# Performance work log

Measured on AMD Instinct MI355X. Metric: run time of the kernel, lower is better.

Reference implementation:

```python
import jax, jax.numpy as jnp
import numpy as np
import math

B, S, KV, D, H = 4, 512, 4096, 1024, 16
HD = D // H  # head_dim = 64


def setup_inputs() -> dict:
    key = jax.random.key(0)
    ks = jax.random.split(key, 12)
    scale = 0.02
    return {
        "x": jax.random.normal(ks[0], (B, S, D), dtype=jnp.float32),
        "xa": jax.random.normal(ks[1], (B, KV, D), dtype=jnp.float32),
        "Wq": jax.random.normal(ks[2], (D, D), dtype=jnp.float32) * scale,
        "bq": jax.random.normal(ks[3], (D,), dtype=jnp.float32) * scale,
        "Wk": jax.random.normal(ks[4], (D, D), dtype=jnp.float32) * scale,  # key has no bias
        "Wv": jax.random.normal(ks[5], (D, D), dtype=jnp.float32) * scale,
        "bv": jax.random.normal(ks[6], (D,), dtype=jnp.float32) * scale,
        "Wo": jax.random.normal(ks[7], (D, D), dtype=jnp.float32) * scale,
        "bo": jax.random.normal(ks[8], (D,), dtype=jnp.float32) * scale,
        "cache_k": jnp.zeros((B, H, KV, HD), dtype=jnp.float32),
        "cache_v": jnp.zeros((B, H, KV, HD), dtype=jnp.float32),
    }


def reference(x, xa, Wq, bq, Wk, Wv, bv, Wo, bo, cache_k, cache_v):
    bsz, seq_len, _ = x.shape
    kv_len = xa.shape[1]
    # projections (torch nn.Linear convention: y = x @ W^T + b)
    q = (x @ Wq.T + bq).reshape(bsz, seq_len, H, HD).transpose(0, 2, 1, 3)   # [B,H,S,HD]
    k = (xa @ Wk.T).reshape(bsz, kv_len, H, HD).transpose(0, 2, 1, 3)        # [B,H,KV,HD]
    v = (xa @ Wv.T + bv).reshape(bsz, kv_len, H, HD).transpose(0, 2, 1, 3)   # [B,H,KV,HD]
    # prefill path: scatter k/v into positions [0, kv_len) of the cache
    updated_k = cache_k.at[:, :, :kv_len, :].set(k)
    updated_v = cache_v.at[:, :, :kv_len, :].set(v)
    # attention over full cache, fp32 softmax as in the original
    scores = jnp.einsum('bhqd,bhkd->bhqk', q, updated_k) / math.sqrt(HD)
    probs = jax.nn.softmax(scores.astype(jnp.float32), axis=-1).astype(q.dtype)
    attn = jnp.einsum('bhqk,bhkd->bhqd', probs, updated_v)                   # [B,H,S,HD]
    attn = attn.transpose(0, 2, 1, 3).reshape(bsz, seq_len, H * HD)
    out = attn @ Wo.T + bo
    return out, updated_k, updated_v
```

## Files before the change

kernel.cpp:

```cpp
#include <hip/hip_runtime.h>
#include <hip/hip_bf16.h>

using u16 = unsigned short;
typedef __bf16 bf16x8 __attribute__((ext_vector_type(8)));
typedef float f32x4 __attribute__((ext_vector_type(4)));

#define SB 4
#define SS 512
#define SKV 4096
#define SD 1024
#define SH 16
#define SHD 64
#define NSPLIT 4
#define NROWS 32768

__device__ inline u16 f2bf(float f){
  __hip_bfloat16 h = __float2bfloat16(f);
  return __builtin_bit_cast(u16, h);
}

__device__ inline bf16x8 ld_frag_g(const u16* p){
  uint4 v = *reinterpret_cast<const uint4*>(p);
  return __builtin_bit_cast(bf16x8, v);
}

__device__ inline bf16x8 ld_frag_lds(const char* base, int ob){
  uint4 v = *reinterpret_cast<const uint4*>(base + ob);
  return __builtin_bit_cast(bf16x8, v);
}

__device__ inline void gload_lds16(const u16* g, u16* l){
  __builtin_amdgcn_global_load_lds(
      (const __attribute__((address_space(1))) void*)g,
      (__attribute__((address_space(3))) void*)l, 16, 0, 0);
}

__global__ __launch_bounds__(256) void cast_kernel(const float* __restrict__ src,
                                                   u16* __restrict__ dst, int n4){
  int i = blockIdx.x * 256 + threadIdx.x;
  if (i < n4){
    float4 f = reinterpret_cast<const float4*>(src)[i];
    ushort4 u;
    u.x = f2bf(f.x); u.y = f2bf(f.y); u.z = f2bf(f.z); u.w = f2bf(f.w);
    reinterpret_cast<ushort4*>(dst)[i] = u;
  }
}

enum { MODE_Q = 0, MODE_K = 1, MODE_V = 2, MODE_OUT = 3 };

template<int MODE>
__global__ __launch_bounds__(256) void gemm_bt(const u16* __restrict__ A,
                                               const u16* __restrict__ W,
                                               const float* __restrict__ bias,
                                               float* __restrict__ outF,
                                               u16* __restrict__ outB)
{
  __shared__ u16 As[128*64];
  __shared__ u16 Bs[128*64];
  const int tid  = threadIdx.x;
  const int lane = tid & 63;
  const int wm   = ((tid >> 6) >> 1) * 64;
  const int wn   = ((tid >> 6) & 1) * 64;
  const long rowBase = (long)blockIdx.x * 128;
  const long colBase = (long)blockIdx.y * 128;

  f32x4 acc[4][4];
#pragma unroll
  for (int i = 0; i < 4; i++)
#pragma unroll
    for (int j = 0; j < 4; j++)
      acc[i][j] = (f32x4){0.f, 0.f, 0.f, 0.f};

  for (int kt = 0; kt < 16; ++kt){
    __syncthreads();
#pragma unroll
    for (int i = 0; i < 4; i++){
      int u = tid + i * 256;
      int r = u >> 3, c = u & 7;
      const u16* ga = A + (rowBase + r) * 1024 + kt * 64 + c * 8;
      const u16* gw = W + (colBase + r) * 1024 + kt * 64 + c * 8;
      u16* la = As + (long)(i * 256 + (tid & ~63)) * 8;
      u16* lw = Bs + (long)(i * 256 + (tid & ~63)) * 8;
      gload_lds16(ga, la);
      gload_lds16(gw, lw);
    }
    __syncthreads();
#pragma unroll
    for (int kk = 0; kk < 2; kk++){
      bf16x8 af[4], bfr[4];
#pragma unroll
      for (int mi = 0; mi < 4; mi++){
        int row = wm + mi * 16 + (lane & 15);
        int ob = row * 128 + kk * 64 + (lane >> 4) * 16;
        af[mi] = __builtin_bit_cast(bf16x8,
                 *reinterpret_cast<const uint4*>(reinterpret_cast<const char*>(As) + ob));
      }
#pragma unroll
      for (int ni = 0; ni < 4; ni++){
        int row = wn + ni * 16 + (lane & 15);
        int ob = row * 128 + kk * 64 + (lane >> 4) * 16;
        bfr[ni] = __builtin_bit_cast(bf16x8,
                 *reinterpret_cast<const uint4*>(reinterpret_cast<const char*>(Bs) + ob));
      }
#pragma unroll
      for (int mi = 0; mi < 4; mi++)
#pragma unroll
        for (int ni = 0; ni < 4; ni++)
          acc[mi][ni] = __builtin_amdgcn_mfma_f32_16x16x32_bf16(af[mi], bfr[ni], acc[mi][ni], 0, 0, 0);
    }
  }

#pragma unroll
  for (int mi = 0; mi < 4; mi++){
#pragma unroll
    for (int ni = 0; ni < 4; ni++){
      long gn = colBase + wn + ni * 16 + (lane & 15);
      float bb = 0.f;
      if (MODE == MODE_Q || MODE == MODE_V || MODE == MODE_OUT) bb = bias[gn];
      if (MODE == MODE_V){
        long gmBase = rowBase + wm + mi * 16 + ((lane >> 4) << 2);
        long b = gmBase >> 12, kv = gmBase & 4095;
        long h = gn >> 6, hd = gn & 63;
        long fidx = ((b * SH + h) * SKV + kv) * SHD + hd;
        ushort4 pk;
        float v0 = acc[mi][ni][0] + bb; outF[fidx          ] = v0; pk.x = f2bf(v0);
        float v1 = acc[mi][ni][1] + bb; outF[fidx +     SHD] = v1; pk.y = f2bf(v1);
        float v2 = acc[mi][ni][2] + bb; outF[fidx + 2 * SHD] = v2; pk.z = f2bf(v2);
        float v3 = acc[mi][ni][3] + bb; outF[fidx + 3 * SHD] = v3; pk.w = f2bf(v3);
        *reinterpret_cast<ushort4*>(outB + ((b * SH + h) * SHD + hd) * SKV + kv) = pk;
      } else {
#pragma unroll
        for (int r = 0; r < 4; r++){
          long gm = rowBase + wm + mi * 16 + ((lane >> 4) << 2) + r;
          float val = acc[mi][ni][r] + bb;
          if (MODE == MODE_OUT){
            outF[gm * 1024 + gn] = val;
          } else if (MODE == MODE_Q){
            long b = gm >> 9, s = gm & 511;
            long h = gn >> 6, hd = gn & 63;
            outB[((b * SH + h) * SS + s) * SHD + hd] = f2bf(val * 0.125f);
          } else {
            long b = gm >> 12, kv = gm & 4095;
            long h = gn >> 6, hd = gn & 63;
            long idx = ((b * SH + h) * SKV + kv) * SHD + hd;
            outF[idx] = val;
            outB[idx] = f2bf(val);
          }
        }
      }
    }
  }
}

__global__ __launch_bounds__(256) void attn_partial(const u16* __restrict__ qb,
                                                    const u16* __restrict__ kb,
                                                    const u16* __restrict__ vTb,
                                                    float* __restrict__ opart,
                                                    float* __restrict__ ml){
  __shared__ u16 Klds[64 * 64];
  __shared__ u16 Vlds[64 * 64];
  __shared__ u16 PT[4][16 * 72];
  const int tid  = threadIdx.x;
  const int lane = tid & 63;
  const int wid  = tid >> 6;
  const int c    = lane & 15;
  const int hi   = lane >> 4;
  const long bh  = blockIdx.x;
  const int  qt  = blockIdx.y;
  const int  split = blockIdx.z;

  const u16* qp = qb + (bh * SS + qt * 64 + wid * 16 + c) * SHD + hi * 8;
  const bf16x8 bq0 = ld_frag_g(qp);
  const bf16x8 bq1 = ld_frag_g(qp + 32);

  f32x4 acc[4];
#pragma unroll
  for (int i = 0; i < 4; i++) acc[i] = (f32x4){0.f, 0.f, 0.f, 0.f};
  float mrun = -INFINITY, lrun = 0.f;

  const u16* kbase = kb  + bh * SKV * SHD;
  const u16* vbase = vTb + bh * SHD * SKV;
  u16* pt = &PT[wid][0];
  char* kch = reinterpret_cast<char*>(Klds);
  char* vch = reinterpret_cast<char*>(Vlds);

  for (int kt = split * 16; kt < split * 16 + 16; ++kt){
    __syncthreads();
#pragma unroll
    for (int i = 0; i < 2; i++){
      int u = tid + i * 256;
      int r = u >> 3, cc = u & 7;
      uint4 kv4 = *reinterpret_cast<const uint4*>(kbase + (kt * 64 + r) * SHD + cc * 8);
      uint4 vv4 = *reinterpret_cast<const uint4*>(vbase + (long)r * SKV + kt * 64 + cc * 8);
      int ob = (r * 128 + cc * 16) ^ ((r & 7) << 4);
      *reinterpret_cast<uint4*>(kch + ob) = kv4;
      *reinterpret_cast<uint4*>(vch + ob) = vv4;
    }
    __syncthreads();

    f32x4 sT[4];
#pragma unroll
    for (int ni = 0; ni < 4; ni++){
      int krow = ni * 16 + c;
      int swz = (krow & 7) << 4;
      int a0 = (krow * 128 + hi * 16) ^ swz;
      int a1 = (krow * 128 + 64 + hi * 16) ^ swz;
      f32x4 z = (f32x4){0.f, 0.f, 0.f, 0.f};
      sT[ni] = __builtin_amdgcn_mfma_f32_16x16x32_bf16(ld_frag_lds(kch, a0), bq0, z, 0, 0, 0);
      sT[ni] = __builtin_amdgcn_mfma_f32_16x16x32_bf16(ld_frag_lds(kch, a1), bq1, sT[ni], 0, 0, 0);
    }
    f32x4 mv = __builtin_elementwise_max(__builtin_elementwise_max(sT[0], sT[1]),
                                         __builtin_elementwise_max(sT[2], sT[3]));
    float t = fmaxf(fmaxf(mv[0], mv[1]), fmaxf(mv[2], mv[3]));
    t = fmaxf(t, __shfl_xor(t, 16));
    t = fmaxf(t, __shfl_xor(t, 32));
    float mn = fmaxf(mrun, t);
    float al = __expf(mrun - mn);
    f32x4 psv = (f32x4){0.f, 0.f, 0.f, 0.f};
#pragma unroll
    for (int ni = 0; ni < 4; ni++){
      f32x4 p;
      p[0] = __expf(sT[ni][0] - mn); p[1] = __expf(sT[ni][1] - mn);
      p[2] = __expf(sT[ni][2] - mn); p[3] = __expf(sT[ni][3] - mn);
      psv += p;
      ushort4 pk;
      pk.x = f2bf(p[0]); pk.y = f2bf(p[1]); pk.z = f2bf(p[2]); pk.w = f2bf(p[3]);
      *reinterpret_cast<ushort4*>(pt + c * 72 + ni * 16 + hi * 4) = pk;
    }
    float ps = (psv[0] + psv[1]) + (psv[2] + psv[3]);
    ps += __shfl_xor(ps, 16);
    ps += __shfl_xor(ps, 32);
    lrun = lrun * al + ps;
    mrun = mn;
#pragma unroll
    for (int ni = 0; ni < 4; ni++) acc[ni] *= al;
#pragma unroll
    for (int m = 0; m < 2; m++){
      bf16x8 pfrag = __builtin_bit_cast(bf16x8,
          *reinterpret_cast<const uint4*>(pt + c * 72 + m * 32 + hi * 8));
#pragma unroll
      for (int ni = 0; ni < 4; ni++){
        int vrow = ni * 16 + c;
        int av = (vrow * 128 + m * 64 + hi * 16) ^ ((vrow & 7) << 4);
        acc[ni] = __builtin_amdgcn_mfma_f32_16x16x32_bf16(ld_frag_lds(vch, av), pfrag, acc[ni], 0, 0, 0);
      }
    }
  }

  const long row = bh * SS + (long)qt * 64 + wid * 16 + c;
  float* ob = opart + ((long)split * NROWS + row) * SHD;
#pragma unroll
  for (int ni = 0; ni < 4; ni++)
    *reinterpret_cast<f32x4*>(ob + ni * 16 + hi * 4) = acc[ni];
  if (hi == 0){
    ml[(long)split * NROWS + row] = mrun;
    ml[(long)NSPLIT * NROWS + (long)split * NROWS + row] = lrun;
  }
}

__global__ __launch_bounds__(256) void attn_combine(const float* __restrict__ opart,
                                                    const float* __restrict__ ml,
                                                    u16* __restrict__ attnb){
  long idx4 = (long)blockIdx.x * 256 + threadIdx.x;
  long row = idx4 >> 4;
  int  c   = (int)(idx4 & 15);
  float m0 = ml[row], m1 = ml[NROWS + row], m2 = ml[2L*NROWS + row], m3 = ml[3L*NROWS + row];
  float M = fmaxf(fmaxf(m0, m1), fmaxf(m2, m3));
  float w0 = __expf(m0 - M), w1 = __expf(m1 - M), w2 = __expf(m2 - M), w3 = __expf(m3 - M);
  const float* lb = ml + (long)NSPLIT * NROWS;
  float L = w0*lb[row] + w1*lb[NROWS+row] + w2*lb[2L*NROWS+row] + w3*lb[3L*NROWS+row];
  float inv = 1.f / L;
  const float4* op = reinterpret_cast<const float4*>(opart);
  float4 v0 = op[(0L*NROWS + row) * 16 + c];
  float4 v1 = op[(1L*NROWS + row) * 16 + c];
  float4 v2 = op[(2L*NROWS + row) * 16 + c];
  float4 v3 = op[(3L*NROWS + row) * 16 + c];
  float4 val;
  val.x = (w0*v0.x + w1*v1.x + w2*v2.x + w3*v3.x) * inv;
  val.y = (w0*v0.y + w1*v1.y + w2*v2.y + w3*v3.y) * inv;
  val.z = (w0*v0.z + w1*v1.z + w2*v2.z + w3*v3.z) * inv;
  val.w = (w0*v0.w + w1*v1.w + w2*v2.w + w3*v3.w) * inv;
  long bh = row >> 9, s = row & 511;
  long b = bh >> 4, h = bh & 15;
  ushort4 u;
  u.x = f2bf(val.x); u.y = f2bf(val.y); u.z = f2bf(val.z); u.w = f2bf(val.w);
  reinterpret_cast<ushort4*>(attnb)[((b * SS + s) * SD + h * SHD) / 4 + c] = u;
}

extern "C" void kernel_launch(void* const* d_in, const int* in_sizes, int n_in,
                              void* d_out, int out_size, void* d_ws, size_t ws_size,
                              hipStream_t stream)
{
  const float* x  = (const float*)d_in[0];
  const float* xa = (const float*)d_in[1];
  const float* Wq = (const float*)d_in[2];
  const float* bq = (const float*)d_in[3];
  const float* Wk = (const float*)d_in[4];
  const float* Wv = (const float*)d_in[5];
  const float* bv = (const float*)d_in[6];
  const float* Wo = (const float*)d_in[7];
  const float* bo = (const float*)d_in[8];

  float* outO = (float*)d_out;
  float* outK = outO + (long)SB * SS * SD;
  float* outV = outK + (long)SB * SH * SKV * SHD;

  u16* ws   = (u16*)d_ws;
  u16* xb   = ws;
  u16* xab  = xb   + 2097152L;
  u16* Wqb  = xab  + 16777216L;
  u16* Wkb  = Wqb  + 1048576L;
  u16* Wvb  = Wkb  + 1048576L;
  u16* Wob  = Wvb  + 1048576L;
  u16* qbuf = Wob  + 1048576L;
  u16* kbuf = qbuf + 2097152L;
  u16* vTbuf= kbuf + 16777216L;
  u16* mlb  = vTbuf+ 16777216L;

  u16*   attnb = xb;
  float* opart = (float*)xab;
  float* ml    = (float*)mlb;

  auto cast_launch = [&](const float* s, u16* d, long n){
    int n4 = (int)(n / 4);
    cast_kernel<<<(n4 + 255) / 256, 256, 0, stream>>>(s, d, n4);
  };
  cast_launch(x,  xb,  2097152L);
  cast_launch(xa, xab, 16777216L);
  cast_launch(Wq, Wqb, 1048576L);
  cast_launch(Wk, Wkb, 1048576L);
  cast_launch(Wv, Wvb, 1048576L);
  cast_launch(Wo, Wob, 1048576L);

  gemm_bt<MODE_Q>  <<<dim3(16, 8),  256, 0, stream>>>(xb,  Wqb, bq, nullptr, qbuf);
  gemm_bt<MODE_K>  <<<dim3(128, 8), 256, 0, stream>>>(xab, Wkb, nullptr, outK, kbuf);
  gemm_bt<MODE_V>  <<<dim3(128, 8), 256, 0, stream>>>(xab, Wvb, bv, outV, vTbuf);
  attn_partial     <<<dim3(64, 8, NSPLIT), 256, 0, stream>>>(qbuf, kbuf, vTbuf, opart, ml);
  attn_combine     <<<2048, 256, 0, stream>>>(opart, ml, attnb);
  gemm_bt<MODE_OUT><<<dim3(16, 8),  256, 0, stream>>>(attnb, Wob, bo, outO, nullptr);
}
```

Measured before the change: 287.5 us.

## Store GEMM tiles in MFMA fragment order and fold log2e into Q scale

The GEMM now loads global data straight into LDS in MFMA fragment order, so each lane reads its fragment at a contiguous lane*16 offset. This removes LDS bank conflicts from the row-major 128-byte-stride reads and precomputes the global load pointers outside the k loop. Separately, Q is scaled by log2(e)/sqrt(64), which lets the attention softmax and the split-combine use exp2f in place of __expf and drops a multiply per exponential. Global loads are now 16-row by 64-byte pieces rather than full 128-byte row segments, which may coalesce less well.

```diff
diff --git a/kernel.cpp b/kernel.cpp
--- a/kernel.cpp
+++ b/kernel.cpp
@@ -13,6 +13,7 @@
 #define SHD 64
 #define NSPLIT 4
 #define NROWS 32768
+#define QSCALE 0.18033688011112042f
 
 __device__ inline u16 f2bf(float f){
   __hip_bfloat16 h = __float2bfloat16(f);
@@ -59,11 +60,22 @@
   __shared__ u16 Bs[128*64];
   const int tid  = threadIdx.x;
   const int lane = tid & 63;
-  const int wm   = ((tid >> 6) >> 1) * 64;
-  const int wn   = ((tid >> 6) & 1) * 64;
+  const int wid  = tid >> 6;
+  const int l15  = lane & 15;
+  const int lhi  = lane >> 4;
+  const int wm   = (wid >> 1) * 64;
+  const int wn   = (wid & 1) * 64;
   const long rowBase = (long)blockIdx.x * 128;
   const long colBase = (long)blockIdx.y * 128;
 
+  const u16* gaB[4]; const u16* gwB[4];
+#pragma unroll
+  for (int i = 0; i < 4; i++){
+    int f = i * 4 + wid, g = f >> 1, kk = f & 1;
+    gaB[i] = A + (rowBase + g * 16 + l15) * 1024 + kk * 32 + lhi * 8;
+    gwB[i] = W + (colBase + g * 16 + l15) * 1024 + kk * 32 + lhi * 8;
+  }
+
   f32x4 acc[4][4];
 #pragma unroll
   for (int i = 0; i < 4; i++)
@@ -75,14 +87,9 @@
     __syncthreads();
 #pragma unroll
     for (int i = 0; i < 4; i++){
-      int u = tid + i * 256;
-      int r = u >> 3, c = u & 7;
-      const u16* ga = A + (rowBase + r) * 1024 + kt * 64 + c * 8;
-      const u16* gw = W + (colBase + r) * 1024 + kt * 64 + c * 8;
-      u16* la = As + (long)(i * 256 + (tid & ~63)) * 8;
-      u16* lw = Bs + (long)(i * 256 + (tid & ~63)) * 8;
-      gload_lds16(ga, la);
-      gload_lds16(gw, lw);
+      int f = i * 4 + wid;
+      gload_lds16(gaB[i] + kt * 64, As + f * 512);
+      gload_lds16(gwB[i] + kt * 64, Bs + f * 512);
     }
     __syncthreads();
 #pragma unroll
@@ -90,17 +97,13 @@
       bf16x8 af[4], bfr[4];
 #pragma unroll
       for (int mi = 0; mi < 4; mi++){
-        int row = wm + mi * 16 + (lane & 15);
-        int ob = row * 128 + kk * 64 + (lane >> 4) * 16;
-        af[mi] = __builtin_bit_cast(bf16x8,
-                 *reinterpret_cast<const uint4*>(reinterpret_cast<const char*>(As) + ob));
+        int fA = ((wm >> 4) + mi) * 2 + kk;
+        af[mi] = ld_frag_lds(reinterpret_cast<const char*>(As), fA * 1024 + lane * 16);
       }
 #pragma unroll
       for (int ni = 0; ni < 4; ni++){
-        int row = wn + ni * 16 + (lane & 15);
-        int ob = row * 128 + kk * 64 + (lane >> 4) * 16;
-        bfr[ni] = __builtin_bit_cast(bf16x8,
-                 *reinterpret_cast<const uint4*>(reinterpret_cast<const char*>(Bs) + ob));
+        int fB = ((wn >> 4) + ni) * 2 + kk;
+        bfr[ni] = ld_frag_lds(reinterpret_cast<const char*>(Bs), fB * 1024 + lane * 16);
       }
 #pragma unroll
       for (int mi = 0; mi < 4; mi++)
@@ -138,7 +141,7 @@
           } else if (MODE == MODE_Q){
             long b = gm >> 9, s = gm & 511;
             long h = gn >> 6, hd = gn & 63;
-            outB[((b * SH + h) * SS + s) * SHD + hd] = f2bf(val * 0.125f);
+            outB[((b * SH + h) * SS + s) * SHD + hd] = f2bf(val * QSCALE);
           } else {
             long b = gm >> 12, kv = gm & 4095;
             long h = gn >> 6, hd = gn & 63;
@@ -215,13 +218,13 @@
     t = fmaxf(t, __shfl_xor(t, 16));
     t = fmaxf(t, __shfl_xor(t, 32));
     float mn = fmaxf(mrun, t);
-    float al = __expf(mrun - mn);
+    float al = exp2f(mrun - mn);
     f32x4 psv = (f32x4){0.f, 0.f, 0.f, 0.f};
 #pragma unroll
     for (int ni = 0; ni < 4; ni++){
       f32x4 p;
-      p[0] = __expf(sT[ni][0] - mn); p[1] = __expf(sT[ni][1] - mn);
-      p[2] = __expf(sT[ni][2] - mn); p[3] = __expf(sT[ni][3] - mn);
+      p[0] = exp2f(sT[ni][0] - mn); p[1] = exp2f(sT[ni][1] - mn);
+      p[2] = exp2f(sT[ni][2] - mn); p[3] = exp2f(sT[ni][3] - mn);
       psv += p;
       ushort4 pk;
       pk.x = f2bf(p[0]); pk.y = f2bf(p[1]); pk.z = f2bf(p[2]); pk.w = f2bf(p[3]);
@@ -266,7 +269,7 @@
   int  c   = (int)(idx4 & 15);
   float m0 = ml[row], m1 = ml[NROWS + row], m2 = ml[2L*NROWS + row], m3 = ml[3L*NROWS + row];
   float M = fmaxf(fmaxf(m0, m1), fmaxf(m2, m3));
-  float w0 = __expf(m0 - M), w1 = __expf(m1 - M), w2 = __expf(m2 - M), w3 = __expf(m3 - M);
+  float w0 = exp2f(m0 - M), w1 = exp2f(m1 - M), w2 = exp2f(m2 - M), w3 = exp2f(m3 - M);
   const float* lb = ml + (long)NSPLIT * NROWS;
   float L = w0*lb[row] + w1*lb[NROWS+row] + w2*lb[2L*NROWS+row] + w3*lb[3L*NROWS+row];
   float inv = 1.f / L;
```

Measured after the change: 330.5 us. +14.9%, slower.
